# Optimization experiments

Hardware: AMD Instinct MI355X
Metric: run time of the kernel (lower is better)

The kernel has to match this reference:

```python
import jax, jax.numpy as jnp
import numpy as np

NUM_HEADS = 16
EPS = 1e-12  # matches torch F.normalize eps


def _l2norm(t):
    n = jnp.sqrt(jnp.sum(t * t, axis=-1, keepdims=True))
    return t / jnp.maximum(n, EPS)


def setup_inputs() -> dict:
    key = jax.random.key(0)
    kx, kq, kk, kv = jax.random.split(key, 4)
    B, S, E = 2, 2048, 1024
    head_dim = E // NUM_HEADS
    bound = 1.0 / np.sqrt(E)  # nn.Linear default init range
    x = jax.random.normal(kx, (B, S, E), dtype=jnp.float32)
    Wq = jax.random.uniform(kq, (E, E), dtype=jnp.float32, minval=-bound, maxval=bound)
    Wk = jax.random.uniform(kk, (E, E), dtype=jnp.float32, minval=-bound, maxval=bound)
    Wv = jax.random.uniform(kv, (E, E), dtype=jnp.float32, minval=-bound, maxval=bound)
    g_scale = jnp.asarray(np.sqrt(head_dim), dtype=jnp.float32)  # 1/d_k = sqrt(head_dim)
    return {"x": x, "Wq": Wq, "Wk": Wk, "Wv": Wv, "g_scale": g_scale}


def reference(x, Wq, Wk, Wv, g_scale):
    B, S, E = x.shape
    H = NUM_HEADS
    D = E // H
    # projections (torch Linear: x @ W.T), split heads -> [B, H, S, D]
    q = (x @ Wq.T).reshape(B, S, H, D).transpose(0, 2, 1, 3)
    k = (x @ Wk.T).reshape(B, S, H, D).transpose(0, 2, 1, 3)
    v = (x @ Wv.T).reshape(B, S, H, D).transpose(0, 2, 1, 3)
    # qk_norm branch: L2-normalize q, k then learnable scale
    q = _l2norm(q)
    k = _l2norm(k)
    scores = g_scale * jnp.einsum('bhqd,bhkd->bhqk', q, k)  # [B, H, S, S]
    attn = jax.nn.softmax(scores, axis=-1)
    # dropout p=0.0 (eval) -> identity
    out = jnp.einsum('bhqk,bhkd->bhqd', attn, v)  # [B, H, S, D]
    out = out.transpose(0, 2, 1, 3).reshape(B, S, E)
    return out
```

## Files before the change

kernel.cpp:

```cpp
#include <hip/hip_runtime.h>
#include <math.h>

#define NH 16
#define HD 64
#define SEQ 2048
#define BAT 2
#define EMB 1024
#define MTOT (BAT*SEQ)
#define NTOT (3*EMB)

typedef __attribute__((ext_vector_type(8))) short bf16x8;
typedef __attribute__((ext_vector_type(4))) float f32x4;

#define MFMA16(a,b,c) __builtin_amdgcn_mfma_f32_16x16x32_bf16(a,b,c,0,0,0)

__device__ inline short f2bf(float f) {
    union { float f; unsigned u; } x; x.f = f;
    unsigned r = (x.u + 0x7FFF + ((x.u >> 16) & 1)) >> 16;
    return (short)r;
}

__device__ inline float fast_exp2(float x) {
#if __has_builtin(__builtin_amdgcn_exp2f)
    return __builtin_amdgcn_exp2f(x);
#else
    float r; asm("v_exp_f32 %0, %1" : "=v"(r) : "v"(x)); return r;
#endif
}

__device__ inline unsigned pack2bf_t(float a, float b) {
    union { float f; unsigned u; } x, y; x.f = a; y.f = b;
    return __builtin_amdgcn_perm(y.u, x.u, 0x07060302u);
}

typedef const __attribute__((address_space(1))) void* gp_t;
typedef __attribute__((address_space(3))) void* lp_t;
__device__ inline void gload16(const void* g, void* l) {
    __builtin_amdgcn_global_load_lds((gp_t)(uintptr_t)g, (lp_t)(uintptr_t)l, 16, 0, 0);
}

__global__ __launch_bounds__(256) void prep_kernel(
    const float* __restrict__ x, const float* __restrict__ wq,
    const float* __restrict__ wk, const float* __restrict__ wv,
    short* __restrict__ xb, short* __restrict__ wb)
{
    const size_t NX = (size_t)MTOT * EMB;
    const size_t NW = (size_t)EMB * EMB;
    const size_t i4 = ((size_t)blockIdx.x * 256 + threadIdx.x) * 4;
    float4 v; short* dst;
    if (i4 < NX) { v = *(const float4*)(x + i4); dst = xb + i4; }
    else {
        size_t j = i4 - NX;
        const float* s = (j < NW) ? wq : (j < 2 * NW) ? wk : wv;
        v = *(const float4*)(s + (j & (NW - 1)));
        dst = wb + j;
    }
    short4 o; o.x = f2bf(v.x); o.y = f2bf(v.y); o.z = f2bf(v.z); o.w = f2bf(v.w);
    *(short4*)dst = o;
}

__global__ __launch_bounds__(256) void qkv_gemm_fast(
    const short* __restrict__ xb, const short* __restrict__ wb,
    short* __restrict__ qws, short* __restrict__ kws, short* __restrict__ vperm,
    const float* __restrict__ gptr)
{
    __shared__ short smem[2 * 2 * 128 * 64];
    const int m0 = blockIdx.x * 128, n0 = blockIdx.y * 128;
    const int t = threadIdx.x, wave = t >> 6, lane = t & 63;
    const int quad = lane >> 4, l16 = lane & 15;
    const int wm = (wave & 1) * 64, wn = (wave >> 1) * 64;

    const int srow = wave * 32 + (lane >> 3);
    const int scol = ((lane & 7) ^ (srow & 7)) * 8;
    const short* ga = xb + (size_t)(m0 + srow) * EMB + scol;
    const short* gb = wb + (size_t)(n0 + srow) * EMB + scol;

    int aoff[2], boff[2];
#pragma unroll
    for (int ks = 0; ks < 2; ++ks) {
        const int pc = (ks * 32 + quad * 8) ^ ((l16 & 7) * 8);
        aoff[ks] = (wm + l16) * 64 + pc;
        boff[ks] = 8192 + (wn + l16) * 64 + pc;
    }

    f32x4 acc[4][4] = {};

    auto stageg = [&](int k0, int p) {
        short* lA = smem + p * 16384 + wave * 2048;
        short* lB = smem + p * 16384 + 8192 + wave * 2048;
#pragma unroll
        for (int j = 0; j < 4; ++j) {
            gload16(ga + k0 + (size_t)j * 8 * EMB, lA + j * 512);
            gload16(gb + k0 + (size_t)j * 8 * EMB, lB + j * 512);
        }
    };

    stageg(0, 0);
    __syncthreads();

    for (int it = 0; it < EMB / 64; ++it) {
        const int p = it & 1;
        if (it + 1 < EMB / 64) stageg((it + 1) * 64, p ^ 1);
        const short* base = smem + p * 16384;
#pragma unroll
        for (int ks = 0; ks < 2; ++ks) {
            bf16x8 af[4], bfr[4];
#pragma unroll
            for (int i = 0; i < 4; ++i) af[i]  = *(const bf16x8*)(base + aoff[ks] + i * 1024);
#pragma unroll
            for (int i = 0; i < 4; ++i) bfr[i] = *(const bf16x8*)(base + boff[ks] + i * 1024);
#pragma unroll
            for (int mf = 0; mf < 4; ++mf)
#pragma unroll
                for (int nf = 0; nf < 4; ++nf)
                    acc[mf][nf] = MFMA16(af[mf], bfr[nf], acc[mf][nf]);
        }
        __syncthreads();
    }

    short* T = smem;
    const int mat = n0 >> 10;

    if (mat < 2) {
        const float scale = (mat == 0) ? gptr[0] * 1.4426950408889634f : 1.0f;
        float inv[4][4];
#pragma unroll
        for (int mf = 0; mf < 4; ++mf)
#pragma unroll
            for (int reg = 0; reg < 4; ++reg) {
                float ss = 0.f;
#pragma unroll
                for (int nf = 0; nf < 4; ++nf) { float v = acc[mf][nf][reg]; ss += v * v; }
                ss += __shfl_xor(ss, 1, 16);
                ss += __shfl_xor(ss, 2, 16);
                ss += __shfl_xor(ss, 4, 16);
                ss += __shfl_xor(ss, 8, 16);
                inv[mf][reg] = scale / fmaxf(sqrtf(ss), 1e-12f);
            }
#pragma unroll
        for (int mf = 0; mf < 4; ++mf)
#pragma unroll
            for (int nf = 0; nf < 4; ++nf) {
                const int c = wn + nf * 16 + l16;
#pragma unroll
                for (int reg = 0; reg < 4; ++reg) {
                    const int s = wm + mf * 16 + quad * 4 + reg;
                    T[s * 128 + (((c >> 3) ^ (s & 15)) << 3) + (c & 7)] =
                        f2bf(acc[mf][nf][reg] * inv[mf][reg]);
                }
            }
        __syncthreads();
        short* outp = (mat == 0) ? qws : kws;
        const int r = t >> 1, half = t & 1;
        const int sg = m0 + r, bb = sg >> 11, sl = sg & (SEQ - 1);
        const int h = ((n0 & 1023) >> 6) + half;
        short* orow = outp + ((size_t)(bb * NH + h) * SEQ + sl) * HD;
#pragma unroll
        for (int j = 0; j < 8; ++j) {
            int4 v = *(const int4*)&T[r * 128 + ((((half * 8 + j)) ^ (r & 15)) << 3)];
            *(int4*)&orow[j * 8] = v;
        }
    } else {
#pragma unroll
        for (int mf = 0; mf < 4; ++mf)
#pragma unroll
            for (int nf = 0; nf < 4; ++nf) {
                const int c = wn + nf * 16 + l16;
#pragma unroll
                for (int reg = 0; reg < 4; ++reg) {
                    const int s = wm + mf * 16 + quad * 4 + reg;
                    const int sp = (s & ~31) + ((s & 12) >> 2) * 8 + ((s >> 4) & 1) * 4 + (s & 3);
                    T[sp * 128 + (((c >> 3) ^ (sp & 15)) << 3) + (c & 7)] =
                        f2bf(acc[mf][nf][reg]);
                }
            }
        __syncthreads();
        const int c = t >> 1, half = t & 1;
        const int h = ((n0 & 1023) >> 6) + (c >> 6), d = c & 63;
        const int bb = m0 >> 11, p0 = (m0 & (SEQ - 1)) + half * 64;
        short* vrow = vperm + ((size_t)(bb * NH + h) * HD + d) * SEQ + p0;
        const int cg = c >> 3, ce = c & 7;
#pragma unroll
        for (int j = 0; j < 8; ++j) {
            union { int4 v; short s[8]; } tmp;
#pragma unroll
            for (int e = 0; e < 8; ++e) {
                const int s = half * 64 + j * 8 + e;
                tmp.s[e] = T[s * 128 + ((cg ^ (s & 15)) << 3) + ce];
            }
            *(int4*)&vrow[j * 8] = tmp.v;
        }
    }
}

__global__ __launch_bounds__(256, 4) void attn_kernel(
    const short* __restrict__ qws, const short* __restrict__ kws,
    const short* __restrict__ vperm, float* __restrict__ out)
{
    __shared__ short Kt[2][2][2048];
    __shared__ short Vt[2][2][2048];
    __shared__ float lbuf[64];

    const int id = blockIdx.x;
    const int bh = (id & 7) * 4 + ((id >> 3) & 3);
    const int qt = id >> 5;
    const int b = bh >> 4, h = bh & (NH - 1);
    const size_t base = (size_t)bh * SEQ * HD;
    const int t = threadIdx.x, wave = t >> 6, lane = t & 63;
    const int quad = lane >> 4, l16 = lane & 15;
    const int qh = wave >> 1, kh = wave & 1;

    bf16x8 bq[2][2];
#pragma unroll
    for (int qsub = 0; qsub < 2; ++qsub) {
        const short* qp = qws + base +
            (size_t)(qt * 64 + qh * 32 + qsub * 16 + l16) * HD + quad * 8;
        bq[qsub][0] = *(const bf16x8*)(qp);
        bq[qsub][1] = *(const bf16x8*)(qp + 32);
    }
    bf16x8 ones;
#pragma unroll
    for (int i = 0; i < 8; ++i) ones[i] = (short)0x3F80;

    int koff[2][2];
#pragma unroll
    for (int msub = 0; msub < 2; ++msub)
#pragma unroll
        for (int ks = 0; ks < 2; ++ks)
            koff[msub][ks] = (msub * 16 + l16) * 64 + (((ks * 4 + quad) ^ (l16 & 7)) * 8);
    int voff[4];
#pragma unroll
    for (int nt = 0; nt < 4; ++nt) {
        const int d = nt * 16 + l16;
        voff[nt] = d * 32 + ((quad ^ ((d >> 1) & 3)) * 8);
    }

    f32x4 o_acc[2][4] = {};
    f32x4 l_acc[2] = {};

    auto stage = [&](int tt, int p) {
        if (qh == 0) {
#pragma unroll
            for (int j = 0; j < 4; ++j) {
                const int kl = j * 8 + (lane >> 3);
                const int row = tt * 64 + kh * 32 + kl;
                gload16(kws + base + (size_t)row * HD + (((lane & 7) ^ (kl & 7)) * 8),
                        &Kt[p][kh][j * 512 + lane * 8]);
            }
        } else {
#pragma unroll
            for (int j = 0; j < 4; ++j) {
                const int d = j * 16 + (lane >> 2);
                const int ug = (lane & 3) ^ ((d >> 1) & 3);
                gload16(vperm + base + (size_t)d * SEQ + tt * 64 + kh * 32 + ug * 8,
                        &Vt[p][kh][j * 512 + lane * 8]);
            }
        }
    };

    stage(0, 0);
    __syncthreads();

    for (int tt = 0; tt < SEQ / 64; ++tt) {
        const int p = tt & 1;
        if (tt + 1 < SEQ / 64) stage(tt + 1, p ^ 1);
        const short* Kp = &Kt[p][kh][0];
        const short* Vp = &Vt[p][kh][0];

        f32x4 st[2][2];
#pragma unroll
        for (int msub = 0; msub < 2; ++msub) {
            bf16x8 a0 = *(const bf16x8*)(Kp + koff[msub][0]);
            bf16x8 a1 = *(const bf16x8*)(Kp + koff[msub][1]);
#pragma unroll
            for (int qsub = 0; qsub < 2; ++qsub) {
                f32x4 z = {};
                z = MFMA16(a0, bq[qsub][0], z);
                st[msub][qsub] = MFMA16(a1, bq[qsub][1], z);
            }
        }
        bf16x8 vf[4];
#pragma unroll
        for (int nt = 0; nt < 4; ++nt)
            vf[nt] = *(const bf16x8*)(Vp + voff[nt]);
#pragma unroll
        for (int qsub = 0; qsub < 2; ++qsub) {
            bf16x8 pa;
            unsigned* pu = (unsigned*)&pa;
            pu[0] = pack2bf_t(fast_exp2(st[0][qsub][0]), fast_exp2(st[0][qsub][1]));
            pu[1] = pack2bf_t(fast_exp2(st[0][qsub][2]), fast_exp2(st[0][qsub][3]));
            pu[2] = pack2bf_t(fast_exp2(st[1][qsub][0]), fast_exp2(st[1][qsub][1]));
            pu[3] = pack2bf_t(fast_exp2(st[1][qsub][2]), fast_exp2(st[1][qsub][3]));
            l_acc[qsub] = MFMA16(pa, ones, l_acc[qsub]);
#pragma unroll
            for (int nt = 0; nt < 4; ++nt)
                o_acc[qsub][nt] = MFMA16(pa, vf[nt], o_acc[qsub][nt]);
        }
        __syncthreads();
    }

    float* red = (float*)&Kt[0][0][0];
    if (kh == 1) {
#pragma unroll
        for (int qsub = 0; qsub < 2; ++qsub) {
#pragma unroll
            for (int nt = 0; nt < 4; ++nt)
#pragma unroll
                for (int r = 0; r < 4; ++r)
                    red[qh * 2048 + (qsub * 16 + quad * 4 + r) * 64 + nt * 16 + l16] =
                        o_acc[qsub][nt][r];
            if (l16 == 0)
#pragma unroll
                for (int r = 0; r < 4; ++r)
                    lbuf[qh * 32 + qsub * 16 + quad * 4 + r] = l_acc[qsub][r];
        }
    }
    __syncthreads();
    if (kh == 0) {
#pragma unroll
        for (int qsub = 0; qsub < 2; ++qsub) {
            float linv[4];
#pragma unroll
            for (int r = 0; r < 4; ++r)
                linv[r] = 1.0f / (l_acc[qsub][r] + lbuf[qh * 32 + qsub * 16 + quad * 4 + r]);
            const int s = qt * 64 + qh * 32 + qsub * 16 + quad * 4;
            float* ob = out + ((size_t)b * SEQ + s) * EMB + h * HD + l16;
#pragma unroll
            for (int nt = 0; nt < 4; ++nt)
#pragma unroll
                for (int r = 0; r < 4; ++r) {
                    const float o = o_acc[qsub][nt][r] +
                        red[qh * 2048 + (qsub * 16 + quad * 4 + r) * 64 + nt * 16 + l16];
                    ob[(size_t)r * EMB + nt * 16] = o * linv[r];
                }
        }
    }
}

extern "C" void kernel_launch(void* const* d_in, const int* in_sizes, int n_in,
                              void* d_out, int out_size, void* d_ws, size_t ws_size,
                              hipStream_t stream) {
    (void)in_sizes; (void)n_in; (void)out_size; (void)ws_size;
    const float* x  = (const float*)d_in[0];
    const float* Wq = (const float*)d_in[1];
    const float* Wk = (const float*)d_in[2];
    const float* Wv = (const float*)d_in[3];
    const float* g  = (const float*)d_in[4];
    float* out = (float*)d_out;

    const size_t per = (size_t)BAT * NH * SEQ * HD;
    short* qws   = (short*)d_ws;
    short* kws   = qws + per;
    short* vperm = kws + per;

    short* xb = (short*)out;
    short* wb = xb + (size_t)MTOT * EMB;

    prep_kernel<<<7168, 256, 0, stream>>>(x, Wq, Wk, Wv, xb, wb);
    qkv_gemm_fast<<<dim3(MTOT / 128, NTOT / 128), 256, 0, stream>>>(
        xb, wb, qws, kws, vperm, g);
    attn_kernel<<<(SEQ / 64) * BAT * NH, 256, 0, stream>>>(qws, kws, vperm, out);
}
```

Baseline: 163.5 us.

## Rewrite QKV GEMM as 256x256 tile, 8-wave ping-pong pipelined kernel

The QKV projection GEMM moves from 128x128 tiles with 4 waves to 256x256 tiles with 8 waves. The K loop is split into four MFMA phases, each with staggered quarter-tile global-to-LDS loads, explicit s_barrier and waitcnt placement, and s_setprio around the MFMA bursts. Blocks are remapped with an XCD-aware swizzle, and the epilogues are adapted to the larger tile. The intent is more operand reuse per LDS load and overlap of memory with MFMA. The cost is higher register and LDS pressure (128 KB LDS) and fragile hand-written synchronisation.

```diff
diff --git a/kernel.cpp b/kernel.cpp
--- a/kernel.cpp
+++ b/kernel.cpp
@@ -8,6 +8,7 @@
 #define EMB 1024
 #define MTOT (BAT*SEQ)
 #define NTOT (3*EMB)
+#define NT (EMB/64)
 
 typedef __attribute__((ext_vector_type(8))) short bf16x8;
 typedef __attribute__((ext_vector_type(4))) float f32x4;
@@ -38,6 +39,25 @@
 __device__ inline void gload16(const void* g, void* l) {
     __builtin_amdgcn_global_load_lds((gp_t)(uintptr_t)g, (lp_t)(uintptr_t)l, 16, 0, 0);
 }
+
+#define BARR() asm volatile("s_barrier" ::: "memory")
+#define VMW(N) asm volatile("s_waitcnt vmcnt(" #N ")" ::: "memory")
+#define LGKM0() asm volatile("s_waitcnt lgkmcnt(0)" ::: "memory")
+
+#define PHASE_MFMA(MH, BB, NHF)                                              \
+    do {                                                                     \
+        __builtin_amdgcn_s_setprio(1);                                       \
+        _Pragma("unroll")                                                    \
+        for (int ks = 0; ks < 2; ++ks)                                       \
+            _Pragma("unroll")                                                \
+            for (int mf4 = 0; mf4 < 4; ++mf4)                                \
+                _Pragma("unroll")                                            \
+                for (int nf2 = 0; nf2 < 2; ++nf2)                            \
+                    acc[(MH)*4 + mf4][(NHF)*2 + nf2] =                       \
+                        MFMA16(af[mf4][ks], BB[nf2][ks],                     \
+                               acc[(MH)*4 + mf4][(NHF)*2 + nf2]);            \
+        __builtin_amdgcn_s_setprio(0);                                       \
+    } while (0)
 
 __global__ __launch_bounds__(256) void prep_kernel(
     const float* __restrict__ x, const float* __restrict__ wq,
@@ -59,63 +79,105 @@
     *(short4*)dst = o;
 }
 
-__global__ __launch_bounds__(256) void qkv_gemm_fast(
+__global__ __launch_bounds__(512, 2) void qkv_gemm_fast(
     const short* __restrict__ xb, const short* __restrict__ wb,
     short* __restrict__ qws, short* __restrict__ kws, short* __restrict__ vperm,
     const float* __restrict__ gptr)
 {
-    __shared__ short smem[2 * 2 * 128 * 64];
-    const int m0 = blockIdx.x * 128, n0 = blockIdx.y * 128;
+    __shared__ short smem[65536];
+
+    const int id = blockIdx.x;
+    const int wg = (id & 7) * 24 + (id >> 3);
+    const int m0 = (wg / 12) * 256;
+    const int n0 = (wg % 12) * 256;
     const int t = threadIdx.x, wave = t >> 6, lane = t & 63;
     const int quad = lane >> 4, l16 = lane & 15;
-    const int wm = (wave & 1) * 64, wn = (wave >> 1) * 64;
-
-    const int srow = wave * 32 + (lane >> 3);
-    const int scol = ((lane & 7) ^ (srow & 7)) * 8;
-    const short* ga = xb + (size_t)(m0 + srow) * EMB + scol;
-    const short* gb = wb + (size_t)(n0 + srow) * EMB + scol;
-
-    int aoff[2], boff[2];
-#pragma unroll
-    for (int ks = 0; ks < 2; ++ks) {
-        const int pc = (ks * 32 + quad * 8) ^ ((l16 & 7) * 8);
-        aoff[ks] = (wm + l16) * 64 + pc;
-        boff[ks] = 8192 + (wn + l16) * 64 + pc;
-    }
-
-    f32x4 acc[4][4] = {};
-
-    auto stageg = [&](int k0, int p) {
-        short* lA = smem + p * 16384 + wave * 2048;
-        short* lB = smem + p * 16384 + 8192 + wave * 2048;
-#pragma unroll
-        for (int j = 0; j < 4; ++j) {
-            gload16(ga + k0 + (size_t)j * 8 * EMB, lA + j * 512);
-            gload16(gb + k0 + (size_t)j * 8 * EMB, lB + j * 512);
-        }
+    const int wr = wave >> 2, wc = wave & 3;
+
+    const int srow8 = lane >> 3;
+    const int sgr = ((lane & 7) ^ srow8) * 8;
+    const short* gA = xb + (size_t)(m0 + wave * 16 + srow8) * EMB + sgr;
+    const short* gB = wb + (size_t)(n0 + wave * 16 + srow8) * EMB + sgr;
+
+    auto stage_half = [&](int kt, int h, int pb) {
+        short* ld = smem + pb * 32768 + h * 8192 + wave * 1024;
+        const short* g = ((h < 2) ? gA + (size_t)(h * 128) * EMB
+                                  : gB + (size_t)((h - 2) * 128) * EMB) + kt * 64;
+        gload16(g, ld);
+        gload16(g + (size_t)8 * EMB, ld + 512);
     };
 
-    stageg(0, 0);
-    __syncthreads();
-
-    for (int it = 0; it < EMB / 64; ++it) {
-        const int p = it & 1;
-        if (it + 1 < EMB / 64) stageg((it + 1) * 64, p ^ 1);
-        const short* base = smem + p * 16384;
-#pragma unroll
-        for (int ks = 0; ks < 2; ++ks) {
-            bf16x8 af[4], bfr[4];
-#pragma unroll
-            for (int i = 0; i < 4; ++i) af[i]  = *(const bf16x8*)(base + aoff[ks] + i * 1024);
-#pragma unroll
-            for (int i = 0; i < 4; ++i) bfr[i] = *(const bf16x8*)(base + boff[ks] + i * 1024);
-#pragma unroll
-            for (int mf = 0; mf < 4; ++mf)
-#pragma unroll
-                for (int nf = 0; nf < 4; ++nf)
-                    acc[mf][nf] = MFMA16(af[mf], bfr[nf], acc[mf][nf]);
-        }
-        __syncthreads();
+    int aoffs[4][2], boffs[4][2];
+#pragma unroll
+    for (int mf4 = 0; mf4 < 4; ++mf4)
+#pragma unroll
+        for (int ks = 0; ks < 2; ++ks)
+            aoffs[mf4][ks] = (mf4 * 16 + l16) * 64 + (((ks * 4 + quad) ^ (l16 & 7)) * 8);
+#pragma unroll
+    for (int nf = 0; nf < 4; ++nf)
+#pragma unroll
+        for (int ks = 0; ks < 2; ++ks)
+            boffs[nf][ks] = ((wc & 1) * 64 + nf * 16 + l16) * 64
+                            + (((ks * 4 + quad) ^ (l16 & 7)) * 8);
+
+    f32x4 acc[8][4] = {};
+    bf16x8 af[4][2], b0[2][2], b1[2][2];
+
+    stage_half(0, 0, 0); stage_half(0, 1, 0); stage_half(0, 2, 0); stage_half(0, 3, 0);
+    stage_half(1, 0, 1);
+    VMW(2);
+    BARR();
+
+#pragma unroll 1
+    for (int kt = 0; kt < NT; ++kt) {
+        const int pp = kt & 1, qq = pp ^ 1;
+        const short* bufA = smem + pp * 32768 + wr * 8192;
+        const short* bufB = smem + pp * 32768 + 16384 + (wc >> 1) * 8192;
+
+#pragma unroll
+        for (int mf4 = 0; mf4 < 4; ++mf4)
+#pragma unroll
+            for (int ks = 0; ks < 2; ++ks)
+                af[mf4][ks] = *(const bf16x8*)(bufA + aoffs[mf4][ks]);
+#pragma unroll
+        for (int nf = 0; nf < 2; ++nf)
+#pragma unroll
+            for (int ks = 0; ks < 2; ++ks)
+                b0[nf][ks] = *(const bf16x8*)(bufB + boffs[nf][ks]);
+        if (kt + 1 < NT) stage_half(kt + 1, 1, qq);
+        BARR();
+        LGKM0();
+        PHASE_MFMA(0, b0, 0);
+        BARR();
+
+#pragma unroll
+        for (int nf = 0; nf < 2; ++nf)
+#pragma unroll
+            for (int ks = 0; ks < 2; ++ks)
+                b1[nf][ks] = *(const bf16x8*)(bufB + boffs[2 + nf][ks]);
+        if (kt + 1 < NT) stage_half(kt + 1, 2, qq);
+        BARR();
+        LGKM0();
+        PHASE_MFMA(0, b1, 1);
+        BARR();
+
+#pragma unroll
+        for (int mf4 = 0; mf4 < 4; ++mf4)
+#pragma unroll
+            for (int ks = 0; ks < 2; ++ks)
+                af[mf4][ks] = *(const bf16x8*)(bufA + 4096 + aoffs[mf4][ks]);
+        if (kt + 1 < NT) stage_half(kt + 1, 3, qq);
+        BARR();
+        LGKM0();
+        PHASE_MFMA(1, b0, 0);
+        BARR();
+
+        if (kt + 2 < NT) stage_half(kt + 2, 0, pp);
+        BARR();
+        PHASE_MFMA(1, b1, 1);
+        if (kt + 2 < NT) { VMW(2); }
+        else             { VMW(0); }
+        BARR();
     }
 
     short* T = smem;
@@ -123,9 +185,9 @@
 
     if (mat < 2) {
         const float scale = (mat == 0) ? gptr[0] * 1.4426950408889634f : 1.0f;
-        float inv[4][4];
-#pragma unroll
-        for (int mf = 0; mf < 4; ++mf)
+#pragma unroll
+        for (int mf = 0; mf < 8; ++mf) {
+            float inv[4];
 #pragma unroll
             for (int reg = 0; reg < 4; ++reg) {
                 float ss = 0.f;
@@ -135,58 +197,59 @@
                 ss += __shfl_xor(ss, 2, 16);
                 ss += __shfl_xor(ss, 4, 16);
                 ss += __shfl_xor(ss, 8, 16);
-                inv[mf][reg] = scale / fmaxf(sqrtf(ss), 1e-12f);
-            }
-#pragma unroll
-        for (int mf = 0; mf < 4; ++mf)
+                inv[reg] = scale / fmaxf(sqrtf(ss), 1e-12f);
+            }
 #pragma unroll
             for (int nf = 0; nf < 4; ++nf) {
-                const int c = wn + nf * 16 + l16;
+                const int c = wc * 64 + nf * 16 + l16;
 #pragma unroll
                 for (int reg = 0; reg < 4; ++reg) {
-                    const int s = wm + mf * 16 + quad * 4 + reg;
-                    T[s * 128 + (((c >> 3) ^ (s & 15)) << 3) + (c & 7)] =
-                        f2bf(acc[mf][nf][reg] * inv[mf][reg]);
+                    const int s = wr * 128 + mf * 16 + quad * 4 + reg;
+                    T[s * 256 + (((c >> 3) ^ (s & 15)) << 3) + (c & 7)] =
+                        f2bf(acc[mf][nf][reg] * inv[reg]);
                 }
             }
+        }
         __syncthreads();
         short* outp = (mat == 0) ? qws : kws;
-        const int r = t >> 1, half = t & 1;
-        const int sg = m0 + r, bb = sg >> 11, sl = sg & (SEQ - 1);
-        const int h = ((n0 & 1023) >> 6) + half;
-        short* orow = outp + ((size_t)(bb * NH + h) * SEQ + sl) * HD;
-#pragma unroll
-        for (int j = 0; j < 8; ++j) {
-            int4 v = *(const int4*)&T[r * 128 + ((((half * 8 + j)) ^ (r & 15)) << 3)];
-            *(int4*)&orow[j * 8] = v;
+        const int i2 = t & 7;
+#pragma unroll
+        for (int it = 0; it < 16; ++it) {
+            const int rh = (t >> 3) + it * 64;
+            const int r = rh >> 2, hq = rh & 3;
+            const int sg = m0 + r, bb = sg >> 11, sl = sg & (SEQ - 1);
+            const int h = ((n0 & 1023) >> 6) + hq;
+            short* orow = outp + ((size_t)(bb * NH + h) * SEQ + sl) * HD;
+            int4 v = *(const int4*)&T[r * 256 + (((hq * 8 + i2) ^ (r & 15)) << 3)];
+            *(int4*)&orow[i2 * 8] = v;
         }
     } else {
 #pragma unroll
-        for (int mf = 0; mf < 4; ++mf)
+        for (int mf = 0; mf < 8; ++mf)
 #pragma unroll
             for (int nf = 0; nf < 4; ++nf) {
-                const int c = wn + nf * 16 + l16;
+                const int c = wc * 64 + nf * 16 + l16;
 #pragma unroll
                 for (int reg = 0; reg < 4; ++reg) {
-                    const int s = wm + mf * 16 + quad * 4 + reg;
+                    const int s = wr * 128 + mf * 16 + quad * 4 + reg;
                     const int sp = (s & ~31) + ((s & 12) >> 2) * 8 + ((s >> 4) & 1) * 4 + (s & 3);
-                    T[sp * 128 + (((c >> 3) ^ (sp & 15)) << 3) + (c & 7)] =
+                    T[sp * 256 + (((c >> 3) ^ (sp & 15)) << 3) + (c & 7)] =
                         f2bf(acc[mf][nf][reg]);
                 }
             }
         __syncthreads();
         const int c = t >> 1, half = t & 1;
         const int h = ((n0 & 1023) >> 6) + (c >> 6), d = c & 63;
-        const int bb = m0 >> 11, p0 = (m0 & (SEQ - 1)) + half * 64;
+        const int bb = m0 >> 11, p0 = (m0 & (SEQ - 1)) + half * 128;
         short* vrow = vperm + ((size_t)(bb * NH + h) * HD + d) * SEQ + p0;
         const int cg = c >> 3, ce = c & 7;
 #pragma unroll
-        for (int j = 0; j < 8; ++j) {
-            union { int4 v; short s[8]; } tmp;
+        for (int j = 0; j < 16; ++j) {
+            union { int4 v; short s8[8]; } tmp;
 #pragma unroll
             for (int e = 0; e < 8; ++e) {
-                const int s = half * 64 + j * 8 + e;
-                tmp.s[e] = T[s * 128 + ((cg ^ (s & 15)) << 3) + ce];
+                const int s = half * 128 + j * 8 + e;
+                tmp.s8[e] = T[s * 256 + ((cg ^ (s & 15)) << 3) + ce];
             }
             *(int4*)&vrow[j * 8] = tmp.v;
         }
@@ -357,7 +420,7 @@
     short* wb = xb + (size_t)MTOT * EMB;
 
     prep_kernel<<<7168, 256, 0, stream>>>(x, Wq, Wk, Wv, xb, wb);
-    qkv_gemm_fast<<<dim3(MTOT / 128, NTOT / 128), 256, 0, stream>>>(
+    qkv_gemm_fast<<<(MTOT / 256) * (NTOT / 256), 512, 0, stream>>>(
         xb, wb, qws, kws, vperm, g);
     attn_kernel<<<(SEQ / 64) * BAT * NH, 256, 0, stream>>>(qws, kws, vperm, out);
 }
```

After: 161.2 us. Within noise of the previous version (-1.4%).

## Give each wave full key tile and double query rows per block

Applied to the files above, without the earlier changes.

The attention kernel now processes 128 query rows per block, with each wave owning 32 query rows and iterating over all 64 keys of the staged tile. Before, the tile was split across two wave pairs by key half. Each loaded K/V tile is reused by twice as many queries, which halves the K/V traffic per query. It also removes the end-of-kernel cross-wave reduction through shared memory and its extra barrier. In exchange the grid is halved to 512 blocks and each wave holds more score registers per iteration, which may lower occupancy or leave CUs less evenly loaded.

```diff
diff --git a/kernel.cpp b/kernel.cpp
--- a/kernel.cpp
+++ b/kernel.cpp
@@ -199,7 +199,6 @@
 {
     __shared__ short Kt[2][2][2048];
     __shared__ short Vt[2][2][2048];
-    __shared__ float lbuf[64];
 
     const int id = blockIdx.x;
     const int bh = (id & 7) * 4 + ((id >> 3) & 3);
@@ -208,13 +207,12 @@
     const size_t base = (size_t)bh * SEQ * HD;
     const int t = threadIdx.x, wave = t >> 6, lane = t & 63;
     const int quad = lane >> 4, l16 = lane & 15;
-    const int qh = wave >> 1, kh = wave & 1;
 
     bf16x8 bq[2][2];
 #pragma unroll
     for (int qsub = 0; qsub < 2; ++qsub) {
         const short* qp = qws + base +
-            (size_t)(qt * 64 + qh * 32 + qsub * 16 + l16) * HD + quad * 8;
+            (size_t)(qt * 128 + wave * 32 + qsub * 16 + l16) * HD + quad * 8;
         bq[qsub][0] = *(const bf16x8*)(qp);
         bq[qsub][1] = *(const bf16x8*)(qp + 32);
     }
@@ -222,12 +220,13 @@
 #pragma unroll
     for (int i = 0; i < 8; ++i) ones[i] = (short)0x3F80;
 
-    int koff[2][2];
-#pragma unroll
-    for (int msub = 0; msub < 2; ++msub)
+    int koff[4][2];
+#pragma unroll
+    for (int msub = 0; msub < 4; ++msub)
 #pragma unroll
         for (int ks = 0; ks < 2; ++ks)
-            koff[msub][ks] = (msub * 16 + l16) * 64 + (((ks * 4 + quad) ^ (l16 & 7)) * 8);
+            koff[msub][ks] = (msub >> 1) * 2048 +
+                ((msub & 1) * 16 + l16) * 64 + (((ks * 4 + quad) ^ (l16 & 7)) * 8);
     int voff[4];
 #pragma unroll
     for (int nt = 0; nt < 4; ++nt) {
@@ -239,21 +238,22 @@
     f32x4 l_acc[2] = {};
 
     auto stage = [&](int tt, int p) {
-        if (qh == 0) {
+        if (wave < 2) {
 #pragma unroll
             for (int j = 0; j < 4; ++j) {
                 const int kl = j * 8 + (lane >> 3);
-                const int row = tt * 64 + kh * 32 + kl;
+                const int row = tt * 64 + wave * 32 + kl;
                 gload16(kws + base + (size_t)row * HD + (((lane & 7) ^ (kl & 7)) * 8),
-                        &Kt[p][kh][j * 512 + lane * 8]);
+                        &Kt[p][wave][j * 512 + lane * 8]);
             }
         } else {
+            const int kv = wave - 2;
 #pragma unroll
             for (int j = 0; j < 4; ++j) {
                 const int d = j * 16 + (lane >> 2);
                 const int ug = (lane & 3) ^ ((d >> 1) & 3);
-                gload16(vperm + base + (size_t)d * SEQ + tt * 64 + kh * 32 + ug * 8,
-                        &Vt[p][kh][j * 512 + lane * 8]);
+                gload16(vperm + base + (size_t)d * SEQ + tt * 64 + kv * 32 + ug * 8,
+                        &Vt[p][kv][j * 512 + lane * 8]);
             }
         }
     };
@@ -264,12 +264,12 @@
     for (int tt = 0; tt < SEQ / 64; ++tt) {
         const int p = tt & 1;
         if (tt + 1 < SEQ / 64) stage(tt + 1, p ^ 1);
-        const short* Kp = &Kt[p][kh][0];
-        const short* Vp = &Vt[p][kh][0];
-
-        f32x4 st[2][2];
-#pragma unroll
-        for (int msub = 0; msub < 2; ++msub) {
+        const short* Kp = &Kt[p][0][0];
+        const short* Vp = &Vt[p][0][0];
+
+        f32x4 st[4][2];
+#pragma unroll
+        for (int msub = 0; msub < 4; ++msub) {
             bf16x8 a0 = *(const bf16x8*)(Kp + koff[msub][0]);
             bf16x8 a1 = *(const bf16x8*)(Kp + koff[msub][1]);
 #pragma unroll
@@ -279,61 +279,42 @@
                 st[msub][qsub] = MFMA16(a1, bq[qsub][1], z);
             }
         }
-        bf16x8 vf[4];
+#pragma unroll
+        for (int s = 0; s < 2; ++s) {
+            bf16x8 vf[4];
+#pragma unroll
+            for (int nt = 0; nt < 4; ++nt)
+                vf[nt] = *(const bf16x8*)(Vp + s * 2048 + voff[nt]);
+#pragma unroll
+            for (int qsub = 0; qsub < 2; ++qsub) {
+                bf16x8 pa;
+                unsigned* pu = (unsigned*)&pa;
+                pu[0] = pack2bf_t(fast_exp2(st[2*s][qsub][0]), fast_exp2(st[2*s][qsub][1]));
+                pu[1] = pack2bf_t(fast_exp2(st[2*s][qsub][2]), fast_exp2(st[2*s][qsub][3]));
+                pu[2] = pack2bf_t(fast_exp2(st[2*s+1][qsub][0]), fast_exp2(st[2*s+1][qsub][1]));
+                pu[3] = pack2bf_t(fast_exp2(st[2*s+1][qsub][2]), fast_exp2(st[2*s+1][qsub][3]));
+                l_acc[qsub] = MFMA16(pa, ones, l_acc[qsub]);
+#pragma unroll
+                for (int nt = 0; nt < 4; ++nt)
+                    o_acc[qsub][nt] = MFMA16(pa, vf[nt], o_acc[qsub][nt]);
+            }
+        }
+        __syncthreads();
+    }
+
+#pragma unroll
+    for (int qsub = 0; qsub < 2; ++qsub) {
+        float linv[4];
+#pragma unroll
+        for (int r = 0; r < 4; ++r)
+            linv[r] = 1.0f / l_acc[qsub][r];
+        const int s = qt * 128 + wave * 32 + qsub * 16 + quad * 4;
+        float* ob = out + ((size_t)b * SEQ + s) * EMB + h * HD + l16;
 #pragma unroll
         for (int nt = 0; nt < 4; ++nt)
-            vf[nt] = *(const bf16x8*)(Vp + voff[nt]);
-#pragma unroll
-        for (int qsub = 0; qsub < 2; ++qsub) {
-            bf16x8 pa;
-            unsigned* pu = (unsigned*)&pa;
-            pu[0] = pack2bf_t(fast_exp2(st[0][qsub][0]), fast_exp2(st[0][qsub][1]));
-            pu[1] = pack2bf_t(fast_exp2(st[0][qsub][2]), fast_exp2(st[0][qsub][3]));
-            pu[2] = pack2bf_t(fast_exp2(st[1][qsub][0]), fast_exp2(st[1][qsub][1]));
-            pu[3] = pack2bf_t(fast_exp2(st[1][qsub][2]), fast_exp2(st[1][qsub][3]));
-            l_acc[qsub] = MFMA16(pa, ones, l_acc[qsub]);
-#pragma unroll
-            for (int nt = 0; nt < 4; ++nt)
-                o_acc[qsub][nt] = MFMA16(pa, vf[nt], o_acc[qsub][nt]);
-        }
-        __syncthreads();
-    }
-
-    float* red = (float*)&Kt[0][0][0];
-    if (kh == 1) {
-#pragma unroll
-        for (int qsub = 0; qsub < 2; ++qsub) {
-#pragma unroll
-            for (int nt = 0; nt < 4; ++nt)
-#pragma unroll
-                for (int r = 0; r < 4; ++r)
-                    red[qh * 2048 + (qsub * 16 + quad * 4 + r) * 64 + nt * 16 + l16] =
-                        o_acc[qsub][nt][r];
-            if (l16 == 0)
-#pragma unroll
-                for (int r = 0; r < 4; ++r)
-                    lbuf[qh * 32 + qsub * 16 + quad * 4 + r] = l_acc[qsub][r];
-        }
-    }
-    __syncthreads();
-    if (kh == 0) {
-#pragma unroll
-        for (int qsub = 0; qsub < 2; ++qsub) {
-            float linv[4];
 #pragma unroll
             for (int r = 0; r < 4; ++r)
-                linv[r] = 1.0f / (l_acc[qsub][r] + lbuf[qh * 32 + qsub * 16 + quad * 4 + r]);
-            const int s = qt * 64 + qh * 32 + qsub * 16 + quad * 4;
-            float* ob = out + ((size_t)b * SEQ + s) * EMB + h * HD + l16;
-#pragma unroll
-            for (int nt = 0; nt < 4; ++nt)
-#pragma unroll
-                for (int r = 0; r < 4; ++r) {
-                    const float o = o_acc[qsub][nt][r] +
-                        red[qh * 2048 + (qsub * 16 + quad * 4 + r) * 64 + nt * 16 + l16];
-                    ob[(size_t)r * EMB + nt * 16] = o * linv[r];
-                }
-        }
+                ob[(size_t)r * EMB + nt * 16] = o_acc[qsub][nt][r] * linv[r];
     }
 }
 
@@ -359,5 +340,5 @@
     prep_kernel<<<7168, 256, 0, stream>>>(x, Wq, Wk, Wv, xb, wb);
     qkv_gemm_fast<<<dim3(MTOT / 128, NTOT / 128), 256, 0, stream>>>(
         xb, wb, qws, kws, vperm, g);
-    attn_kernel<<<(SEQ / 64) * BAT * NH, 256, 0, stream>>>(qws, kws, vperm, out);
-}
+    attn_kernel<<<(SEQ / 128) * BAT * NH, 256, 0, stream>>>(qws, kws, vperm, out);
+}
```

Result: faster. 160.3 us (-2.0%).
